# Performance work log

Measured on AMD Instinct MI355X. Metric: run time of the kernel, lower is better.

The kernel has to match this reference:

```python
import jax, jax.numpy as jnp
import numpy as np

N_NODES = 10000
N_EDGES = 160000
NUM_FEAT = 14
EDGE_DIM = 4
DIM = 64        # hidden_channels
HID = 128       # GENConv MLP expansion = 2
LAYERS = 28
MSG_EPS = 1e-7  # GENConv eps added to relu(message)
LN_EPS = 1e-5   # torch LayerNorm default


def layernorm(h, g, b):
    mu = jnp.mean(h, axis=-1, keepdims=True)
    var = jnp.mean(jnp.square(h - mu), axis=-1, keepdims=True)
    return (h - mu) * jax.lax.rsqrt(var + LN_EPS) * g + b


def gen_conv(x, ea, src, dst, t, W1, b1, g1, be1, W2, b2):
    # message: relu(x_j + edge_attr) + eps  -> [E, D]
    msg = jax.nn.relu(x[src] + ea) + MSG_EPS
    # softmax aggregation over edges grouped by destination node
    logits = msg * t
    m = jax.ops.segment_max(logits, dst, num_segments=N_NODES)
    e = jnp.exp(logits - m[dst])
    s = jax.ops.segment_sum(e, dst, num_segments=N_NODES)
    alpha = e / (s[dst] + 1e-16)
    agg = jax.ops.segment_sum(msg * alpha, dst, num_segments=N_NODES)
    # residual + MLP [D -> 2D -> D] with LayerNorm+ReLU in between
    h = agg + x
    h = jax.nn.relu(layernorm(h @ W1 + b1, g1, be1))
    return h @ W2 + b2


def setup_inputs() -> dict:
    key = jax.random.key(0)
    ks = jax.random.split(key, 24)
    sc = 0.05
    inp = {
        "x": jax.random.normal(ks[0], (N_NODES, NUM_FEAT), jnp.float32),
        "edge_attr": jax.random.normal(ks[1], (N_EDGES, EDGE_DIM), jnp.float32),
        "src": jax.random.randint(ks[2], (N_EDGES,), 0, N_NODES, jnp.int32),
        "dst": jax.random.randint(ks[3], (N_EDGES,), 0, N_NODES, jnp.int32),
        # encoders
        "W_node": jax.random.normal(ks[4], (NUM_FEAT, DIM), jnp.float32) * sc,
        "b_node": jnp.zeros((DIM,), jnp.float32),
        "W_edge": jax.random.normal(ks[5], (EDGE_DIM, DIM), jnp.float32) * sc,
        "b_edge": jnp.zeros((DIM,), jnp.float32),
        # per-layer GENConv params (stacked over LAYERS)
        "t": jnp.ones((LAYERS,), jnp.float32),
        "W1": jax.random.normal(ks[6], (LAYERS, DIM, HID), jnp.float32) * sc,
        "b1": jnp.zeros((LAYERS, HID), jnp.float32),
        "g1": jnp.ones((LAYERS, HID), jnp.float32),
        "be1": jnp.zeros((LAYERS, HID), jnp.float32),
        "W2": jax.random.normal(ks[7], (LAYERS, HID, DIM), jnp.float32) * sc,
        "b2": jnp.zeros((LAYERS, DIM), jnp.float32),
        # per-layer DeepGCNLayer LayerNorm
        "ln_g": jnp.ones((LAYERS, DIM), jnp.float32),
        "ln_b": jnp.zeros((LAYERS, DIM), jnp.float32),
        # output projection
        "W_out": jax.random.normal(ks[8], (DIM, DIM), jnp.float32) * sc,
        "b_out": jnp.zeros((DIM,), jnp.float32),
    }
    return inp


def reference(x, edge_attr, src, dst, W_node, b_node, W_edge, b_edge,
              t, W1, b1, g1, be1, W2, b2, ln_g, ln_b, W_out, b_out):
    h = x @ W_node + b_node                  # node encoder  [N, D]
    ea = edge_attr @ W_edge + b_edge         # edge encoder  [E, D]

    # layer 0: conv only (no res+ wrapper), per DeeperGCN.forward
    h = gen_conv(h, ea, src, dst, t[0], W1[0], b1[0], g1[0], be1[0], W2[0], b2[0])

    # layers 1..L-1: res+ block: x + conv(dropout(relu(norm(x))))  (eval: dropout = id)
    def step(hc, p):
        ti, w1, bb1, gg1, bbe1, w2, bb2, lg, lb = p
        u = jax.nn.relu(layernorm(hc, lg, lb))
        u = gen_conv(u, ea, src, dst, ti, w1, bb1, gg1, bbe1, w2, bb2)
        return hc + u, None

    rest = (t[1:], W1[1:], b1[1:], g1[1:], be1[1:], W2[1:], b2[1:], ln_g[1:], ln_b[1:])
    h, _ = jax.lax.scan(step, h, rest)

    # final: act(layers[0].norm(x)), dropout (eval: id), lin
    h = jax.nn.relu(layernorm(h, ln_g[0], ln_b[0]))
    return h @ W_out + b_out
```

## Files before the change

### kernel.cpp

```cpp
#include <hip/hip_runtime.h>

#define N_NODES 10000
#define N_EDGES 160000
#define NUM_FEAT 14
#define EDGE_DIM 4
#define DIM 64
#define HID 128
#define LAYERS 28

#define NEG_INF (-__builtin_inff())


__global__ __launch_bounds__(256) void k_zero(int* __restrict__ p, int n) {
  int i = blockIdx.x * 256 + threadIdx.x;
  if (i < n) p[i] = 0;
}

__global__ __launch_bounds__(256) void k_hist(const int* __restrict__ dst, int* __restrict__ cur) {
  int e = blockIdx.x * 256 + threadIdx.x;
  if (e < N_EDGES) atomicAdd(&cur[dst[e]], 1);
}

__global__ __launch_bounds__(256) void k_scan(int* __restrict__ cur, int* __restrict__ off) {
  __shared__ int part[256];
  int t = threadIdx.x;
  const int CH = 40;
  int base = t * CH;
  int s = 0;
  for (int i = 0; i < CH; i++) {
    int idx = base + i;
    if (idx < N_NODES) s += cur[idx];
  }
  part[t] = s;
  __syncthreads();
  for (int ofs = 1; ofs < 256; ofs <<= 1) {
    int tmp = (t >= ofs) ? part[t - ofs] : 0;
    __syncthreads();
    part[t] += tmp;
    __syncthreads();
  }
  int run = part[t] - s;
  for (int i = 0; i < CH; i++) {
    int idx = base + i;
    if (idx < N_NODES) {
      int d = cur[idx];
      off[idx] = run;
      cur[idx] = run;
      run += d;
    }
  }
  if (t == 255) off[N_NODES] = part[255];
}

__global__ __launch_bounds__(256) void k_scatter(const int* __restrict__ dst, int* __restrict__ cur,
                                                 int* __restrict__ eids) {
  int e = blockIdx.x * 256 + threadIdx.x;
  if (e < N_EDGES) {
    int p = atomicAdd(&cur[dst[e]], 1);
    eids[p] = e;
  }
}

__global__ __launch_bounds__(256) void k_sortgather(
    const int* __restrict__ off, const int* __restrict__ eids,
    const int* __restrict__ src, const float4* __restrict__ eattr,
    int* __restrict__ src_s, float4* __restrict__ eattr_s) {
  int node = blockIdx.x * 4 + (threadIdx.x >> 6);
  int lane = threadIdx.x & 63;
  if (node >= N_NODES) return;
  int a = off[node];
  int d = off[node + 1] - a;
  if (d <= 64) {
    int key = (lane < d) ? eids[a + lane] : 0x7fffffff;
#pragma unroll
    for (int k = 2; k <= 64; k <<= 1) {
      for (int j = k >> 1; j > 0; j >>= 1) {
        int p = __shfl_xor(key, j);
        bool dirUp = ((lane & k) == 0);
        bool isLower = ((lane & j) == 0);
        key = ((isLower == dirUp) ? min(key, p) : max(key, p));
      }
    }
    if (lane < d) {
      int e = key;
      src_s[a + lane] = src[e];
      eattr_s[a + lane] = eattr[e];
    }
  } else {
    for (int i = lane; i < d; i += 64) {
      int e = eids[a + i];
      int r = 0;
      for (int j = 0; j < d; j++) r += (eids[a + j] < e) ? 1 : 0;
      src_s[a + r] = src[e];
      eattr_s[a + r] = eattr[e];
    }
  }
}


__global__ __launch_bounds__(256) void k_ea(const float4* __restrict__ eattr_s,
                                            const float* __restrict__ W_edge,
                                            const float* __restrict__ b_edge,
                                            float* __restrict__ ea_s) {
  int gid = blockIdx.x * 256 + threadIdx.x;
  if (gid >= N_EDGES * 64) return;
  int slot = gid >> 6, f = gid & 63;
  float4 ev = eattr_s[slot];
  ea_s[gid] = b_edge[f] + ev.x * W_edge[f] + ev.y * W_edge[64 + f] +
              ev.z * W_edge[128 + f] + ev.w * W_edge[192 + f];
}


__global__ __launch_bounds__(256) void k_enc(const float* __restrict__ x, const float* __restrict__ Wn,
                                             const float* __restrict__ bn, float* __restrict__ hc,
                                             float* __restrict__ u) {
  int gid = blockIdx.x * 256 + threadIdx.x;
  if (gid >= N_NODES * DIM) return;
  int n = gid >> 6, j = gid & 63;
  float acc = bn[j];
#pragma unroll
  for (int k = 0; k < NUM_FEAT; k++) acc += x[n * NUM_FEAT + k] * Wn[k * DIM + j];
  hc[gid] = acc;
  u[gid] = acc;
}


template <bool GUARD>
__device__ __forceinline__ void agg8(
    const int* __restrict__ src_s, const float* __restrict__ ea_s,
    const float* __restrict__ uin, int base, int rem, int lane, float tv,
    float& m, float& sum, float& acc) {
  float uv[8], ev[8];
#pragma unroll
  for (int j = 0; j < 8; j++) {
    if (!GUARD || j < rem) {
      int sn = src_s[base + j];
      uv[j] = uin[(sn << 6) + lane];
      ev[j] = ea_s[((base + j) << 6) + lane];
    }
  }
  float msg[8], lg[8];
#pragma unroll
  for (int j = 0; j < 8; j++) {
    if (!GUARD || j < rem) {
      float mv = fmaxf(uv[j] + ev[j], 0.f) + 1e-7f;
      msg[j] = mv;
      lg[j] = mv * tv;
    } else {
      msg[j] = 0.f;
      lg[j] = NEG_INF;
    }
  }
  float t4[4];
#pragma unroll
  for (int j = 0; j < 4; j++) t4[j] = fmaxf(lg[j], lg[j + 4]);
  float bm = fmaxf(fmaxf(t4[0], t4[1]), fmaxf(t4[2], t4[3]));
  float es[8];
#pragma unroll
  for (int j = 0; j < 8; j++) es[j] = __expf(lg[j] - bm);
  float ss[4], aa[4];
#pragma unroll
  for (int j = 0; j < 4; j++) {
    ss[j] = es[j] + es[j + 4];
    aa[j] = es[j] * msg[j] + es[j + 4] * msg[j + 4];
  }
  float sB = (ss[0] + ss[1]) + (ss[2] + ss[3]);
  float aB = (aa[0] + aa[1]) + (aa[2] + aa[3]);
  float mn = fmaxf(m, bm);
  float sc = __expf(m - mn), sb = __expf(bm - mn);
  sum = sum * sc + sB * sb;
  acc = acc * sc + aB * sb;
  m = mn;
}

__global__ __launch_bounds__(256) void k_edge(
    const float* __restrict__ uin, const float* __restrict__ ea_s,
    const int* __restrict__ src_s, const int* __restrict__ off,
    const float* __restrict__ tptr, int layer, float* __restrict__ htmp) {
  int node = __builtin_amdgcn_readfirstlane((blockIdx.x << 2) + (threadIdx.x >> 6));
  int lane = threadIdx.x & 63;
  float tv = tptr[layer];
  int a = off[node], d = off[node + 1] - a;
  float un = uin[(node << 6) + lane];
  float m = NEG_INF, sum = 0.f, acc = 0.f;
  int nfull = d & ~7;
  for (int i = 0; i < nfull; i += 8)
    agg8<false>(src_s, ea_s, uin, a + i, 8, lane, tv, m, sum, acc);
  int rem = d - nfull;
  if (rem)
    agg8<true>(src_s, ea_s, uin, a + nfull, rem, lane, tv, m, sum, acc);
  htmp[(node << 6) + lane] = acc / (sum + 1e-16f) + un;
}


#define MBLK (N_NODES / 16)

__global__ __launch_bounds__(512, 4) void k_mlp2(
    const float* __restrict__ hin, float* __restrict__ hc, float* __restrict__ uout,
    const float* __restrict__ W1, const float* __restrict__ b1,
    const float* __restrict__ g1, const float* __restrict__ be1,
    const float* __restrict__ W2, const float* __restrict__ b2,
    const float* __restrict__ lng, const float* __restrict__ lnb,
    int addRes, int writeU) {
  __shared__ float sW1[64 * 128];
  __shared__ float sW2[128 * 64];
  __shared__ float sH[8][128];
  __shared__ float sZ[8][256];

  int tid = threadIdx.x;
  int lane = tid & 63;
  int wv = tid >> 6;
  int gn0 = blockIdx.x * 16 + wv * 2;
  int gn1 = gn0 + 1;

  for (int i = tid; i < 2048; i += 512) ((float4*)sW1)[i] = ((const float4*)W1)[i];
  for (int i = tid; i < 2048; i += 512) ((float4*)sW2)[i] = ((const float4*)W2)[i];

  {
    float h0 = hin[gn0 * 64 + lane];
    float h1 = hin[gn1 * 64 + lane];
    *((float2*)&sH[wv][lane * 2]) = make_float2(h0, h1);
  }
  __syncthreads();

  int j0 = 2 * lane;
  float2 b1v = *((const float2*)&b1[j0]);
  float a00 = b1v.x, a01 = b1v.y, a10 = b1v.x, a11 = b1v.y;
#pragma unroll 8
  for (int k = 0; k < 64; k++) {
    float2 hp = *((float2*)&sH[wv][k * 2]);
    float2 wp = *((float2*)&sW1[k * 128 + j0]);
    a00 += hp.x * wp.x; a01 += hp.x * wp.y;
    a10 += hp.y * wp.x; a11 += hp.y * wp.y;
  }

  {
    float2 gv = *((const float2*)&g1[j0]);
    float2 bev = *((const float2*)&be1[j0]);
    float s0 = a00 + a01, q0 = a00 * a00 + a01 * a01;
    float s1 = a10 + a11, q1 = a10 * a10 + a11 * a11;
#pragma unroll
    for (int o = 32; o; o >>= 1) {
      s0 += __shfl_xor(s0, o); q0 += __shfl_xor(q0, o);
      s1 += __shfl_xor(s1, o); q1 += __shfl_xor(q1, o);
    }
    float mu0 = s0 * (1.f / 128.f), mu1 = s1 * (1.f / 128.f);
    float rs0 = rsqrtf(q0 * (1.f / 128.f) - mu0 * mu0 + 1e-5f);
    float rs1 = rsqrtf(q1 * (1.f / 128.f) - mu1 * mu1 + 1e-5f);
    float4 zv;
    zv.x = fmaxf((a00 - mu0) * rs0 * gv.x + bev.x, 0.f);
    zv.y = fmaxf((a10 - mu1) * rs1 * gv.x + bev.x, 0.f);
    zv.z = fmaxf((a01 - mu0) * rs0 * gv.y + bev.y, 0.f);
    zv.w = fmaxf((a11 - mu1) * rs1 * gv.y + bev.y, 0.f);
    *((float4*)&sZ[wv][4 * lane]) = zv;
  }

  float bo = b2[lane];
  float o0 = bo, o1 = bo;
#pragma unroll 8
  for (int k = 0; k < 128; k++) {
    float2 zp = *((float2*)&sZ[wv][k * 2]);
    float wv2 = sW2[k * 64 + lane];
    o0 += zp.x * wv2;
    o1 += zp.y * wv2;
  }

  float r0 = addRes ? hc[gn0 * 64 + lane] : 0.f;
  float r1 = addRes ? hc[gn1 * 64 + lane] : 0.f;
  float hcn0 = o0 + r0, hcn1 = o1 + r1;
  hc[gn0 * 64 + lane] = hcn0;
  hc[gn1 * 64 + lane] = hcn1;

  if (writeU) {
    float lg_ = lng[lane], lb_ = lnb[lane];
    float s0 = hcn0, q0 = hcn0 * hcn0;
    float s1 = hcn1, q1 = hcn1 * hcn1;
#pragma unroll
    for (int o = 32; o; o >>= 1) {
      s0 += __shfl_xor(s0, o); q0 += __shfl_xor(q0, o);
      s1 += __shfl_xor(s1, o); q1 += __shfl_xor(q1, o);
    }
    float mu0 = s0 * (1.f / 64.f), mu1 = s1 * (1.f / 64.f);
    float rs0 = rsqrtf(q0 * (1.f / 64.f) - mu0 * mu0 + 1e-5f);
    float rs1 = rsqrtf(q1 * (1.f / 64.f) - mu1 * mu1 + 1e-5f);
    uout[gn0 * 64 + lane] = fmaxf((hcn0 - mu0) * rs0 * lg_ + lb_, 0.f);
    uout[gn1 * 64 + lane] = fmaxf((hcn1 - mu1) * rs1 * lg_ + lb_, 0.f);
  }
}


__global__ __launch_bounds__(256) void k_final(const float* __restrict__ hc, const float* __restrict__ g,
                                               const float* __restrict__ bptr, const float* __restrict__ Wout,
                                               const float* __restrict__ bout, float* __restrict__ out) {
  __shared__ float sW[DIM * DIM];
  int tid = threadIdx.x;
  for (int i = tid; i < 1024; i += 256) ((float4*)sW)[i] = ((const float4*)Wout)[i];
  __syncthreads();
  int lane = tid & 63, w = tid >> 6;
  int n = blockIdx.x * 4 + w;
  if (n >= N_NODES) return;
  float v = hc[n * 64 + lane];
  float s = v, q = v * v;
#pragma unroll
  for (int o = 32; o; o >>= 1) { s += __shfl_xor(s, o); q += __shfl_xor(q, o); }
  float mu = s * (1.f / 64.f);
  float var = q * (1.f / 64.f) - mu * mu;
  float rs = rsqrtf(var + 1e-5f);
  float z = fmaxf((v - mu) * rs * g[lane] + bptr[lane], 0.f);
  float acc = bout[lane];
  for (int k = 0; k < 64; k++) {
    float zk = __shfl(z, k);
    acc += zk * sW[k * 64 + lane];
  }
  out[n * 64 + lane] = acc;
}


extern "C" void kernel_launch(void* const* d_in, const int* in_sizes, int n_in,
                              void* d_out, int out_size, void* d_ws, size_t ws_size,
                              hipStream_t stream) {
  const float* x        = (const float*)d_in[0];
  const float* eattr    = (const float*)d_in[1];
  const int*   src      = (const int*)d_in[2];
  const int*   dst      = (const int*)d_in[3];
  const float* W_node   = (const float*)d_in[4];
  const float* b_node   = (const float*)d_in[5];
  const float* W_edge   = (const float*)d_in[6];
  const float* b_edge   = (const float*)d_in[7];
  const float* t        = (const float*)d_in[8];
  const float* W1       = (const float*)d_in[9];
  const float* b1       = (const float*)d_in[10];
  const float* g1       = (const float*)d_in[11];
  const float* be1      = (const float*)d_in[12];
  const float* W2       = (const float*)d_in[13];
  const float* b2       = (const float*)d_in[14];
  const float* ln_g     = (const float*)d_in[15];
  const float* ln_b     = (const float*)d_in[16];
  const float* W_out    = (const float*)d_in[17];
  const float* b_out    = (const float*)d_in[18];
  float* out = (float*)d_out;

  char* w = (char*)d_ws;
  float* u       = (float*)w;  w += (size_t)N_NODES * 64 * 4;
  float* hcb     = (float*)w;  w += (size_t)N_NODES * 64 * 4;
  float* htmp    = (float*)w;  w += (size_t)N_NODES * 64 * 4;
  int* off       = (int*)w;    w += (size_t)(N_NODES + 1) * 4;
  int* cur       = (int*)w;    w += (size_t)N_NODES * 4;
  int* eids      = (int*)w;    w += (size_t)N_EDGES * 4;
  int* src_s     = (int*)w;    w += (size_t)N_EDGES * 4;
  float4* eattr_s = (float4*)w; w += (size_t)N_EDGES * 16;
  float* ea_s    = (float*)w;  w += (size_t)N_EDGES * 64 * 4;

  k_zero<<<(N_NODES + 255) / 256, 256, 0, stream>>>(cur, N_NODES);
  k_hist<<<(N_EDGES + 255) / 256, 256, 0, stream>>>(dst, cur);
  k_scan<<<1, 256, 0, stream>>>(cur, off);
  k_scatter<<<(N_EDGES + 255) / 256, 256, 0, stream>>>(dst, cur, eids);
  k_sortgather<<<(N_NODES + 3) / 4, 256, 0, stream>>>(off, eids, src, (const float4*)eattr,
                                                      src_s, eattr_s);
  k_ea<<<(N_EDGES * 64 + 255) / 256, 256, 0, stream>>>((const float4*)eattr_s, W_edge,
                                                       b_edge, ea_s);

  k_enc<<<(N_NODES * 64 + 255) / 256, 256, 0, stream>>>(x, W_node, b_node, hcb, u);

  for (int l = 0; l < LAYERS; l++) {
    k_edge<<<(N_NODES + 3) / 4, 256, 0, stream>>>(u, ea_s, src_s, off, t, l, htmp);
    int nxt = (l + 1 < LAYERS) ? (l + 1) : 0;
    k_mlp2<<<MBLK, 512, 0, stream>>>(htmp, hcb, u,
                                     W1 + (size_t)l * DIM * HID, b1 + (size_t)l * HID,
                                     g1 + (size_t)l * HID, be1 + (size_t)l * HID,
                                     W2 + (size_t)l * HID * DIM, b2 + (size_t)l * DIM,
                                     ln_g + (size_t)nxt * DIM, ln_b + (size_t)nxt * DIM,
                                     (l > 0) ? 1 : 0, (l < LAYERS - 1) ? 1 : 0);
  }

  k_final<<<(N_NODES + 3) / 4, 256, 0, stream>>>(hcb, ln_g, ln_b, W_out, b_out, out);
}
```

Before: 1.004 ms.

## Drop softmax max-shift, fuse edge encoder into sort, stage MLP weights via LDS loads

The edge aggregation drops the running-max rescaling of the segment softmax and instead accumulates exp(msg*t) directly into two interleaved partial sums, removing the per-batch max and rescale exps. The separate edge-encoder kernel is folded into the sort/gather kernel, which computes the 64-wide encoded edge features from shuffled raw attributes. The MLP kernel stages W1 and W2 into shared memory with direct global-to-LDS loads, and a zeroing kernel is replaced by a memset. Skipping the max shift risks exp overflow if logits grow large, and the fused high-degree path reads eattr_s values just written by other lanes without an explicit fence.

```diff
diff --git a/kernel.cpp b/kernel.cpp
--- a/kernel.cpp
+++ b/kernel.cpp
@@ -10,11 +10,12 @@
 
 #define NEG_INF (-__builtin_inff())
 
-
-__global__ __launch_bounds__(256) void k_zero(int* __restrict__ p, int n) {
-  int i = blockIdx.x * 256 + threadIdx.x;
-  if (i < n) p[i] = 0;
-}
+__device__ __forceinline__ void stage16(const float* gsrc, float* lds_base) {
+  __builtin_amdgcn_global_load_lds(
+      (const __attribute__((address_space(1))) void*)gsrc,
+      (__attribute__((address_space(3))) void*)lds_base, 16, 0, 0);
+}
+
 
 __global__ __launch_bounds__(256) void k_hist(const int* __restrict__ dst, int* __restrict__ cur) {
   int e = blockIdx.x * 256 + threadIdx.x;
@@ -64,10 +65,14 @@
 __global__ __launch_bounds__(256) void k_sortgather(
     const int* __restrict__ off, const int* __restrict__ eids,
     const int* __restrict__ src, const float4* __restrict__ eattr,
-    int* __restrict__ src_s, float4* __restrict__ eattr_s) {
+    const float* __restrict__ W_edge, const float* __restrict__ b_edge,
+    int* __restrict__ src_s, float4* __restrict__ eattr_s, float* __restrict__ ea_s) {
   int node = blockIdx.x * 4 + (threadIdx.x >> 6);
   int lane = threadIdx.x & 63;
   if (node >= N_NODES) return;
+  float we0 = W_edge[lane], we1 = W_edge[64 + lane], we2 = W_edge[128 + lane],
+        we3 = W_edge[192 + lane];
+  float be = b_edge[lane];
   int a = off[node];
   int d = off[node + 1] - a;
   if (d <= 64) {
@@ -81,10 +86,16 @@
         key = ((isLower == dirUp) ? min(key, p) : max(key, p));
       }
     }
+    float4 ev = make_float4(0.f, 0.f, 0.f, 0.f);
     if (lane < d) {
-      int e = key;
-      src_s[a + lane] = src[e];
-      eattr_s[a + lane] = eattr[e];
+      src_s[a + lane] = src[key];
+      ev = eattr[key];
+    }
+    for (int j = 0; j < d; j++) {
+      float ex = __shfl(ev.x, j), ey = __shfl(ev.y, j),
+            ez = __shfl(ev.z, j), ew = __shfl(ev.w, j);
+      ea_s[(size_t)(a + j) * 64 + lane] =
+          be + ex * we0 + ey * we1 + ez * we2 + ew * we3;
     }
   } else {
     for (int i = lane; i < d; i += 64) {
@@ -94,20 +105,12 @@
       src_s[a + r] = src[e];
       eattr_s[a + r] = eattr[e];
     }
-  }
-}
-
-
-__global__ __launch_bounds__(256) void k_ea(const float4* __restrict__ eattr_s,
-                                            const float* __restrict__ W_edge,
-                                            const float* __restrict__ b_edge,
-                                            float* __restrict__ ea_s) {
-  int gid = blockIdx.x * 256 + threadIdx.x;
-  if (gid >= N_EDGES * 64) return;
-  int slot = gid >> 6, f = gid & 63;
-  float4 ev = eattr_s[slot];
-  ea_s[gid] = b_edge[f] + ev.x * W_edge[f] + ev.y * W_edge[64 + f] +
-              ev.z * W_edge[128 + f] + ev.w * W_edge[192 + f];
+    for (int j = 0; j < d; j++) {
+      float4 e4 = eattr_s[a + j];
+      ea_s[(size_t)(a + j) * 64 + lane] =
+          be + e4.x * we0 + e4.y * we1 + e4.z * we2 + e4.w * we3;
+    }
+  }
 }
 
 
@@ -124,54 +127,6 @@
   u[gid] = acc;
 }
 
-
-template <bool GUARD>
-__device__ __forceinline__ void agg8(
-    const int* __restrict__ src_s, const float* __restrict__ ea_s,
-    const float* __restrict__ uin, int base, int rem, int lane, float tv,
-    float& m, float& sum, float& acc) {
-  float uv[8], ev[8];
-#pragma unroll
-  for (int j = 0; j < 8; j++) {
-    if (!GUARD || j < rem) {
-      int sn = src_s[base + j];
-      uv[j] = uin[(sn << 6) + lane];
-      ev[j] = ea_s[((base + j) << 6) + lane];
-    }
-  }
-  float msg[8], lg[8];
-#pragma unroll
-  for (int j = 0; j < 8; j++) {
-    if (!GUARD || j < rem) {
-      float mv = fmaxf(uv[j] + ev[j], 0.f) + 1e-7f;
-      msg[j] = mv;
-      lg[j] = mv * tv;
-    } else {
-      msg[j] = 0.f;
-      lg[j] = NEG_INF;
-    }
-  }
-  float t4[4];
-#pragma unroll
-  for (int j = 0; j < 4; j++) t4[j] = fmaxf(lg[j], lg[j + 4]);
-  float bm = fmaxf(fmaxf(t4[0], t4[1]), fmaxf(t4[2], t4[3]));
-  float es[8];
-#pragma unroll
-  for (int j = 0; j < 8; j++) es[j] = __expf(lg[j] - bm);
-  float ss[4], aa[4];
-#pragma unroll
-  for (int j = 0; j < 4; j++) {
-    ss[j] = es[j] + es[j + 4];
-    aa[j] = es[j] * msg[j] + es[j + 4] * msg[j + 4];
-  }
-  float sB = (ss[0] + ss[1]) + (ss[2] + ss[3]);
-  float aB = (aa[0] + aa[1]) + (aa[2] + aa[3]);
-  float mn = fmaxf(m, bm);
-  float sc = __expf(m - mn), sb = __expf(bm - mn);
-  sum = sum * sc + sB * sb;
-  acc = acc * sc + aB * sb;
-  m = mn;
-}
 
 __global__ __launch_bounds__(256) void k_edge(
     const float* __restrict__ uin, const float* __restrict__ ea_s,
@@ -182,13 +137,37 @@
   float tv = tptr[layer];
   int a = off[node], d = off[node + 1] - a;
   float un = uin[(node << 6) + lane];
-  float m = NEG_INF, sum = 0.f, acc = 0.f;
-  int nfull = d & ~7;
-  for (int i = 0; i < nfull; i += 8)
-    agg8<false>(src_s, ea_s, uin, a + i, 8, lane, tv, m, sum, acc);
-  int rem = d - nfull;
-  if (rem)
-    agg8<true>(src_s, ea_s, uin, a + nfull, rem, lane, tv, m, sum, acc);
+  float s0 = 0.f, s1 = 0.f, ac0 = 0.f, ac1 = 0.f;
+  int i = 0;
+  for (; i + 8 <= d; i += 8) {
+    float uv[8], ev[8];
+#pragma unroll
+    for (int j = 0; j < 8; j++) {
+      int sn = src_s[a + i + j];
+      uv[j] = uin[(sn << 6) + lane];
+      ev[j] = ea_s[(size_t)(a + i + j) * 64 + lane];
+    }
+#pragma unroll
+    for (int j = 0; j < 8; j++) {
+      float msg = fmaxf(uv[j] + ev[j], 0.f) + 1e-7f;
+      float e = __expf(msg * tv);
+      if (j & 1) {
+        s1 += e;
+        ac1 = fmaf(e, msg, ac1);
+      } else {
+        s0 += e;
+        ac0 = fmaf(e, msg, ac0);
+      }
+    }
+  }
+  for (; i < d; i++) {
+    int sn = src_s[a + i];
+    float msg = fmaxf(uin[(sn << 6) + lane] + ea_s[(size_t)(a + i) * 64 + lane], 0.f) + 1e-7f;
+    float e = __expf(msg * tv);
+    s0 += e;
+    ac0 = fmaf(e, msg, ac0);
+  }
+  float sum = s0 + s1, acc = ac0 + ac1;
   htmp[(node << 6) + lane] = acc / (sum + 1e-16f) + un;
 }
 
@@ -213,8 +192,17 @@
   int gn0 = blockIdx.x * 16 + wv * 2;
   int gn1 = gn0 + 1;
 
-  for (int i = tid; i < 2048; i += 512) ((float4*)sW1)[i] = ((const float4*)W1)[i];
-  for (int i = tid; i < 2048; i += 512) ((float4*)sW2)[i] = ((const float4*)W2)[i];
+  {
+    const float* w1s = W1 + wv * 1024;
+    const float* w2s = W2 + wv * 1024;
+    float* d1 = sW1 + wv * 1024;
+    float* d2 = sW2 + wv * 1024;
+#pragma unroll
+    for (int r = 0; r < 4; r++) {
+      stage16(w1s + r * 256 + lane * 4, d1 + r * 256);
+      stage16(w2s + r * 256 + lane * 4, d2 + r * 256);
+    }
+  }
 
   {
     float h0 = hin[gn0 * 64 + lane];
@@ -351,14 +339,12 @@
   float4* eattr_s = (float4*)w; w += (size_t)N_EDGES * 16;
   float* ea_s    = (float*)w;  w += (size_t)N_EDGES * 64 * 4;
 
-  k_zero<<<(N_NODES + 255) / 256, 256, 0, stream>>>(cur, N_NODES);
+  hipMemsetAsync(cur, 0, (size_t)N_NODES * 4, stream);
   k_hist<<<(N_EDGES + 255) / 256, 256, 0, stream>>>(dst, cur);
   k_scan<<<1, 256, 0, stream>>>(cur, off);
   k_scatter<<<(N_EDGES + 255) / 256, 256, 0, stream>>>(dst, cur, eids);
   k_sortgather<<<(N_NODES + 3) / 4, 256, 0, stream>>>(off, eids, src, (const float4*)eattr,
-                                                      src_s, eattr_s);
-  k_ea<<<(N_EDGES * 64 + 255) / 256, 256, 0, stream>>>((const float4*)eattr_s, W_edge,
-                                                       b_edge, ea_s);
+                                                      W_edge, b_edge, src_s, eattr_s, ea_s);
 
   k_enc<<<(N_NODES * 64 + 255) / 256, 256, 0, stream>>>(x, W_node, b_node, hcb, u);
 
```

Measured after the change: 988.9 us. No clear change (-1.5%).
